# Performance work log

Measured on AMD Instinct MI355X. Metric: run time of the kernel, lower is better.

The kernel has to match this reference:

```python
import jax, jax.numpy as jnp
import numpy as np
import math

# model / graph sizes
N_NODES, N_EDGES = 50000, 400000
IN_DIM, N_HID = 256, 128
NUM_TYPES, NUM_REL = 4, 5
N_HEADS, D_K = 4, 32
N_LAYERS, MAX_LEN = 2, 240
SQRT_DK = math.sqrt(D_K)


def _gelu(x):
    return jax.nn.gelu(x, approximate=False)  # torch F.gelu is exact erf


def _per_type_linear(x, types, W, b):
    # x:[n,din], types:[n] int, W:[T,din,dout], b:[T,dout]
    out = jnp.zeros((x.shape[0], W.shape[-1]), x.dtype)
    for t in range(W.shape[0]):  # small fixed type count
        out = jnp.where((types == t)[:, None], x @ W[t] + b[t], out)
    return out


def setup_inputs() -> dict:
    key = jax.random.key(0)
    ks = jax.random.split(key, 16)
    node_feature = jax.random.normal(ks[0], (N_NODES, IN_DIM), jnp.float32)
    node_type = jax.random.randint(ks[1], (N_NODES,), 0, NUM_TYPES)
    edge_index = jax.random.randint(ks[2], (2, N_EDGES), 0, N_NODES)
    edge_type = jax.random.randint(ks[3], (N_EDGES,), 0, NUM_REL)
    edge_time = jax.random.randint(ks[4], (N_EDGES,), 0, MAX_LEN)

    def w(k, shape, s=0.05):
        return jax.random.normal(k, shape, jnp.float32) * s

    adapt_W = w(ks[5], (NUM_TYPES, IN_DIM, N_HID))
    adapt_b = jnp.zeros((NUM_TYPES, N_HID), jnp.float32)
    Wk = w(ks[6], (N_LAYERS, NUM_TYPES, N_HID, N_HID))
    Wq = w(ks[7], (N_LAYERS, NUM_TYPES, N_HID, N_HID))
    Wv = w(ks[8], (N_LAYERS, NUM_TYPES, N_HID, N_HID))
    Wa = w(ks[9], (N_LAYERS, NUM_TYPES, N_HID, N_HID))
    bk = jnp.zeros((N_LAYERS, NUM_TYPES, N_HID), jnp.float32)
    bq = jnp.zeros((N_LAYERS, NUM_TYPES, N_HID), jnp.float32)
    bv = jnp.zeros((N_LAYERS, NUM_TYPES, N_HID), jnp.float32)
    ba = jnp.zeros((N_LAYERS, NUM_TYPES, N_HID), jnp.float32)
    rel_pri = jnp.ones((N_LAYERS, NUM_REL, N_HEADS), jnp.float32)
    rel_att = w(ks[10], (N_LAYERS, NUM_REL, N_HEADS, D_K, D_K), 0.1) + jnp.eye(D_K, dtype=jnp.float32)
    rel_msg = w(ks[11], (N_LAYERS, NUM_REL, N_HEADS, D_K, D_K), 0.1) + jnp.eye(D_K, dtype=jnp.float32)
    skip = jnp.ones((N_LAYERS, NUM_TYPES), jnp.float32)
    # fixed sinusoidal RTE table (pyHGT RelTemporalEncoding, requires_grad=False)
    pos = np.arange(MAX_LEN, dtype=np.float32)[:, None]
    div = np.exp(np.arange(0, N_HID, 2, dtype=np.float32) * -(math.log(10000.0) / N_HID))
    tab = np.zeros((MAX_LEN, N_HID), np.float32)
    tab[:, 0::2] = np.sin(pos * div) / math.sqrt(N_HID)
    tab[:, 1::2] = np.cos(pos * div) / math.sqrt(N_HID)
    rte_emb = jnp.asarray(tab)
    rte_W = w(ks[12], (N_LAYERS, N_HID, N_HID))
    rte_b = jnp.zeros((N_LAYERS, N_HID), jnp.float32)
    return dict(node_feature=node_feature, adapt_W=adapt_W, adapt_b=adapt_b,
                Wk=Wk, bk=bk, Wq=Wq, bq=bq, Wv=Wv, bv=bv, Wa=Wa, ba=ba,
                rel_pri=rel_pri, rel_att=rel_att, rel_msg=rel_msg, skip=skip,
                rte_emb=rte_emb, rte_W=rte_W, rte_b=rte_b,
                node_type=node_type, edge_index=edge_index,
                edge_type=edge_type, edge_time=edge_time)


def reference(node_feature, adapt_W, adapt_b, Wk, bk, Wq, bq, Wv, bv, Wa, ba,
              rel_pri, rel_att, rel_msg, skip, rte_emb, rte_W, rte_b,
              node_type, edge_index, edge_type, edge_time):
    n = node_feature.shape[0]
    src, dst = edge_index[0], edge_index[1]  # PyG: row0 = source j, row1 = target i
    st, tt = node_type[src], node_type[dst]
    # per-type input adaptation (all types use Linear + GELU)
    h = _gelu(_per_type_linear(node_feature, node_type, adapt_W, adapt_b))  # [N, n_hid]
    for l in range(N_LAYERS):  # HGTConv stack
        x_j, x_i = h[src], h[dst]
        s_e = x_j + rte_emb[edge_time] @ rte_W[l] + rte_b[l]  # RTE on source per edge
        k = _per_type_linear(s_e, st, Wk[l], bk[l]).reshape(-1, N_HEADS, D_K)
        v = _per_type_linear(s_e, st, Wv[l], bv[l]).reshape(-1, N_HEADS, D_K)
        q = _per_type_linear(x_i, tt, Wq[l], bq[l]).reshape(-1, N_HEADS, D_K)
        att = jnp.zeros((k.shape[0], N_HEADS), h.dtype)
        msg = jnp.zeros_like(v)
        for r in range(NUM_REL):  # small fixed relation count
            m = edge_type == r
            kr = jnp.einsum('ehd,hdk->ehk', k, rel_att[l, r])
            ar = jnp.einsum('ehd,ehd->eh', q, kr) * rel_pri[l, r] / SQRT_DK
            mr = jnp.einsum('ehd,hdk->ehk', v, rel_msg[l, r])
            att = jnp.where(m[:, None], ar, att)
            msg = jnp.where(m[:, None, None], mr, msg)
        # segment softmax over incoming edges of each target node
        amax = jax.lax.stop_gradient(jax.ops.segment_max(att, dst, num_segments=n))
        ex = jnp.exp(att - amax[dst])
        denom = jax.ops.segment_sum(ex, dst, num_segments=n)
        alpha = ex / (denom[dst] + 1e-16)
        aggr = jax.ops.segment_sum((msg * alpha[:, :, None]).reshape(-1, N_HEADS * D_K),
                                   dst, num_segments=n)  # [N, n_hid]
        g = _gelu(aggr)
        res = jnp.zeros_like(h)
        for t in range(NUM_TYPES):  # per-type output transform + gated skip
            a_t = jax.nn.sigmoid(skip[l, t])
            res = jnp.where((node_type == t)[:, None],
                            (g @ Wa[l, t] + ba[l, t]) * a_t + h * (1.0 - a_t), res)
        h = res
    return h
```

## Files before the change

### kernel.cpp

```cpp
#include <hip/hip_runtime.h>
#include <math.h>

#define NN     50000
#define NE     400000
#define INDIM  256
#define NH     128
#define NTYPE  4
#define NREL   5
#define NHEAD  4
#define DK     32
#define RSQRT_DK 0.17677669529663687f
#define BN     64
#define NSCAN_BLK ((NN + 255) / 256)
#define XB     260

__device__ __forceinline__ float gelu_f(float x){
    return 0.5f * x * (1.0f + erff(x * 0.70710678118654752f));
}

__device__ __forceinline__ void gload16(const float* g, float* s){
    __builtin_amdgcn_global_load_lds(
        (const __attribute__((address_space(1))) void*)g,
        (__attribute__((address_space(3))) void*)s, 16, 0, 0);
}

__global__ void GNN_nscatter(const int* __restrict__ ntype, int* __restrict__ ncur,
                             int* __restrict__ nperm){
    __shared__ int lcnt[4], lbase[4];
    int tid = threadIdx.x;
    if (tid < 4) lcnt[tid] = 0;
    __syncthreads();
    int n = blockIdx.x * 256 + tid;
    int t = 0, lpos = 0;
    bool ok = (n < NN);
    if (ok){ t = ntype[n]; lpos = atomicAdd(&lcnt[t], 1); }
    __syncthreads();
    if (tid < 4 && lcnt[tid] > 0) lbase[tid] = atomicAdd(&ncur[tid], lcnt[tid]);
    __syncthreads();
    if (ok) nperm[t * NN + lbase[t] + lpos] = n;
}

__global__ void GNN_deg(const int* __restrict__ edst, int* __restrict__ deg){
    int e = blockIdx.x * 256 + threadIdx.x;
    if (e < NE) atomicAdd(&deg[edst[e]], 1);
}

__global__ void GNN_scan1(const int* __restrict__ deg, int* __restrict__ rowptr,
                          int* __restrict__ bsum){
    __shared__ int s[256];
    int g = blockIdx.x * 256 + threadIdx.x;
    int v = (g < NN) ? deg[g] : 0;
    s[threadIdx.x] = v;
    __syncthreads();
    for (int off = 1; off < 256; off <<= 1){
        int t = (threadIdx.x >= off) ? s[threadIdx.x - off] : 0;
        __syncthreads();
        s[threadIdx.x] += t;
        __syncthreads();
    }
    if (g < NN) rowptr[g] = s[threadIdx.x] - v;
    if (threadIdx.x == 255) bsum[blockIdx.x] = s[255];
}

__global__ void GNN_scan2(const int* __restrict__ bsum, int* __restrict__ bbase){
    __shared__ int s[256];
    int v = (threadIdx.x < NSCAN_BLK) ? bsum[threadIdx.x] : 0;
    s[threadIdx.x] = v;
    __syncthreads();
    for (int off = 1; off < 256; off <<= 1){
        int t = (threadIdx.x >= off) ? s[threadIdx.x - off] : 0;
        __syncthreads();
        s[threadIdx.x] += t;
        __syncthreads();
    }
    bbase[threadIdx.x] = s[threadIdx.x] - v;
}

__global__ void GNN_scan3(int* __restrict__ rowptr, const int* __restrict__ bbase){
    int g = blockIdx.x * 256 + threadIdx.x;
    if (g < NN) rowptr[g] += bbase[blockIdx.x];
    if (g == 0) rowptr[NN] = NE;
}

__global__ void GNN_csr_scatter(const int* __restrict__ edst, const int* __restrict__ rowptr,
                                int* __restrict__ cursor, int* __restrict__ csr_e){
    int e = blockIdx.x * 256 + threadIdx.x;
    if (e >= NE) return;
    int d = edst[e];
    int pos = atomicAdd(&cursor[d], 1);
    csr_e[rowptr[d] + pos] = e;
}

template<int MODE>
__device__ __forceinline__ void gemm_tile(
    const float* __restrict__ X, int K,
    const float* __restrict__ W, const float* __restrict__ brow,
    float a_t, const float* __restrict__ Hprev,
    float* Xs, float* Ws, const int* nids,
    float* __restrict__ OUT)
{
    int tid = threadIdx.x;
    int cq = tid & 31, rq = tid >> 5;

    int xc0 = tid >> 6,          xr0i = tid & 63;
    int xc1 = (256 + tid) >> 6,  xr1i = tid & 63;
    int nid0 = nids[xr0i], nid1 = nids[xr1i];
    const float* xp0 = (nid0 >= 0) ? X + (size_t)nid0 * K + xc0 * 4 : nullptr;
    const float* xp1 = (nid1 >= 0) ? X + (size_t)nid1 * K + xc1 * 4 : nullptr;
    int wk = tid >> 5, wc4 = (tid & 31) * 4;

    float4 xr0, xr1, wr0, wr1, wr2, wr3;
    const float4 z4 = make_float4(0.f, 0.f, 0.f, 0.f);

    #define LOADREGS(k0)                                                        \
        xr0 = xp0 ? *(const float4*)(xp0 + (k0)) : z4;                          \
        xr1 = xp1 ? *(const float4*)(xp1 + (k0)) : z4;                          \
        wr0 = *(const float4*)(W + (size_t)((k0) + wk     ) * NH + wc4);        \
        wr1 = *(const float4*)(W + (size_t)((k0) + wk +  8) * NH + wc4);        \
        wr2 = *(const float4*)(W + (size_t)((k0) + wk + 16) * NH + wc4);        \
        wr3 = *(const float4*)(W + (size_t)((k0) + wk + 24) * NH + wc4);

    #define WRITELDS()                                                          \
        *(float4*)&Xs[xc0 * XB + xr0i * 4] = xr0;                               \
        *(float4*)&Xs[xc1 * XB + xr1i * 4] = xr1;                               \
        *(float4*)&Ws[(wk     ) * 128 + wc4] = wr0;                             \
        *(float4*)&Ws[(wk +  8) * 128 + wc4] = wr1;                             \
        *(float4*)&Ws[(wk + 16) * 128 + wc4] = wr2;                             \
        *(float4*)&Ws[(wk + 24) * 128 + wc4] = wr3;

    float acc[8][4];
    #pragma unroll
    for (int i = 0; i < 8; i++){ acc[i][0]=0.f; acc[i][1]=0.f; acc[i][2]=0.f; acc[i][3]=0.f; }

    LOADREGS(0);
    for (int k0 = 0; k0 < K; k0 += 32){
        WRITELDS();
        __syncthreads();
        if (k0 + 32 < K){ LOADREGS(k0 + 32); }
        #pragma unroll 2
        for (int c4 = 0; c4 < 8; c4++){
            float4 w0 = *(const float4*)&Ws[(c4*4+0)*128 + cq*4];
            float4 w1 = *(const float4*)&Ws[(c4*4+1)*128 + cq*4];
            float4 w2 = *(const float4*)&Ws[(c4*4+2)*128 + cq*4];
            float4 w3 = *(const float4*)&Ws[(c4*4+3)*128 + cq*4];
            #pragma unroll
            for (int i = 0; i < 8; i++){
                float4 xv = *(const float4*)&Xs[c4 * XB + (rq + 8*i) * 4];
                acc[i][0] += xv.x*w0.x + xv.y*w1.x + xv.z*w2.x + xv.w*w3.x;
                acc[i][1] += xv.x*w0.y + xv.y*w1.y + xv.z*w2.y + xv.w*w3.y;
                acc[i][2] += xv.x*w0.z + xv.y*w1.z + xv.z*w2.z + xv.w*w3.z;
                acc[i][3] += xv.x*w0.w + xv.y*w1.w + xv.z*w2.w + xv.w*w3.w;
            }
        }
        __syncthreads();
    }
    #undef LOADREGS
    #undef WRITELDS

    float4 b4 = *(const float4*)(brow + cq * 4);
    float one_m = 1.f - a_t;
    #pragma unroll
    for (int i = 0; i < 8; i++){
        int r = rq + 8*i;
        int nid = nids[r];
        if (nid < 0) continue;
        float v0 = acc[i][0] + b4.x, v1 = acc[i][1] + b4.y;
        float v2 = acc[i][2] + b4.z, v3 = acc[i][3] + b4.w;
        if (MODE == 0){ v0 = gelu_f(v0); v1 = gelu_f(v1); v2 = gelu_f(v2); v3 = gelu_f(v3); }
        if (MODE == 2){
            float4 hp = *(const float4*)(Hprev + (size_t)nid * NH + cq * 4);
            v0 = v0 * a_t + hp.x * one_m; v1 = v1 * a_t + hp.y * one_m;
            v2 = v2 * a_t + hp.z * one_m; v3 = v3 * a_t + hp.w * one_m;
        }
        *(float4*)(OUT + (size_t)nid * NH + cq * 4) = make_float4(v0, v1, v2, v3);
    }
}

template<int MODE>
__device__ __forceinline__ void gemm_tile_dma(
    const float* __restrict__ X, int K,
    const float* __restrict__ W, const float* __restrict__ brow,
    float a_t, const float* __restrict__ Hprev,
    float* Xs, float* Ws, const int* nids,
    float* __restrict__ OUT)
{
    int tid = threadIdx.x;
    int cq = tid & 31, rq = tid >> 5;
    int lane = tid & 63, w = tid >> 6;

    int nidl = nids[lane]; if (nidl < 0) nidl = 0;
    const float* xrow  = X + (size_t)nidl * K;
    const float* wbase = W + lane * 4;

    float acc[8][4];
    #pragma unroll
    for (int i = 0; i < 8; i++){ acc[i][0]=0.f; acc[i][1]=0.f; acc[i][2]=0.f; acc[i][3]=0.f; }

    #define STAGE(k0, Xb, Wb)                                                   \
        gload16(xrow + (k0) + w * 4,       (Xb) + w * 256);                     \
        gload16(xrow + (k0) + (w + 4) * 4, (Xb) + (w + 4) * 256);               \
        gload16(wbase + (size_t)((k0) + 2 * (w     )) * NH, (Wb) + (w     ) * 256); \
        gload16(wbase + (size_t)((k0) + 2 * (w +  4)) * NH, (Wb) + (w +  4) * 256); \
        gload16(wbase + (size_t)((k0) + 2 * (w +  8)) * NH, (Wb) + (w +  8) * 256); \
        gload16(wbase + (size_t)((k0) + 2 * (w + 12)) * NH, (Wb) + (w + 12) * 256);

    STAGE(0, Xs, Ws);
    int buf = 0;
    for (int k0 = 0; k0 < K; k0 += 32){
        __syncthreads();
        if (k0 + 32 < K){
            float* Xn = Xs + (buf ^ 1) * 2048;
            float* Wn = Ws + (buf ^ 1) * 4096;
            STAGE(k0 + 32, Xn, Wn);
        }
        const float* Xsb = Xs + buf * 2048;
        const float* Wsb = Ws + buf * 4096;
        #pragma unroll 2
        for (int c4 = 0; c4 < 8; c4++){
            float4 w0 = *(const float4*)&Wsb[(c4*4+0)*128 + cq*4];
            float4 w1 = *(const float4*)&Wsb[(c4*4+1)*128 + cq*4];
            float4 w2 = *(const float4*)&Wsb[(c4*4+2)*128 + cq*4];
            float4 w3 = *(const float4*)&Wsb[(c4*4+3)*128 + cq*4];
            #pragma unroll
            for (int i = 0; i < 8; i++){
                float4 xv = *(const float4*)&Xsb[c4 * 256 + (rq + 8*i) * 4];
                acc[i][0] += xv.x*w0.x + xv.y*w1.x + xv.z*w2.x + xv.w*w3.x;
                acc[i][1] += xv.x*w0.y + xv.y*w1.y + xv.z*w2.y + xv.w*w3.y;
                acc[i][2] += xv.x*w0.z + xv.y*w1.z + xv.z*w2.z + xv.w*w3.z;
                acc[i][3] += xv.x*w0.w + xv.y*w1.w + xv.z*w2.w + xv.w*w3.w;
            }
        }
        __syncthreads();
        buf ^= 1;
    }
    #undef STAGE

    float4 b4 = *(const float4*)(brow + cq * 4);
    float one_m = 1.f - a_t;
    #pragma unroll
    for (int i = 0; i < 8; i++){
        int r = rq + 8*i;
        int nid = nids[r];
        if (nid < 0) continue;
        float v0 = acc[i][0] + b4.x, v1 = acc[i][1] + b4.y;
        float v2 = acc[i][2] + b4.z, v3 = acc[i][3] + b4.w;
        if (MODE == 0){ v0 = gelu_f(v0); v1 = gelu_f(v1); v2 = gelu_f(v2); v3 = gelu_f(v3); }
        if (MODE == 2){
            float4 hp = *(const float4*)(Hprev + (size_t)nid * NH + cq * 4);
            v0 = v0 * a_t + hp.x * one_m; v1 = v1 * a_t + hp.y * one_m;
            v2 = v2 * a_t + hp.z * one_m; v3 = v3 * a_t + hp.w * one_m;
        }
        *(float4*)(OUT + (size_t)nid * NH + cq * 4) = make_float4(v0, v1, v2, v3);
    }
}

template<int MODE>
__global__ __launch_bounds__(256) void GNN_ptype_gemm(
    const float* __restrict__ X, int K,
    const float* __restrict__ Wall, const float* __restrict__ ball,
    const float* __restrict__ skiprow, const float* __restrict__ Hprev,
    const int* __restrict__ nperm, const int* __restrict__ counts,
    float* __restrict__ OUT)
{
    int t = blockIdx.y;
    int cnt = counts[t];
    int rbase = blockIdx.x * BN;
    if (rbase >= cnt) return;
    __shared__ float Xs[2 * 2048];
    __shared__ float Ws[2 * 4096];
    __shared__ int nids[BN];
    int tid = threadIdx.x;
    if (tid < BN){
        int idx = rbase + tid;
        nids[tid] = (idx < cnt) ? nperm[t * NN + idx] : -1;
    }
    __syncthreads();
    float a_t = 0.f;
    if (MODE == 2) a_t = 1.f / (1.f + expf(-skiprow[t]));
    gemm_tile_dma<MODE>(X, K, Wall + (size_t)t * K * NH, ball + t * NH,
                        a_t, Hprev, Xs, Ws, nids, OUT);
}

__global__ __launch_bounds__(256) void GNN_qkv_gemm(
    const float* __restrict__ X,
    const float* __restrict__ Wq, const float* __restrict__ bq,
    const float* __restrict__ Wk, const float* __restrict__ bk,
    const float* __restrict__ Wv, const float* __restrict__ bv,
    const int* __restrict__ nperm, const int* __restrict__ counts,
    float* __restrict__ Qn, float* __restrict__ Kn, float* __restrict__ Vn)
{
    int t = blockIdx.y;
    int cnt = counts[t];
    int rbase = blockIdx.x * BN;
    if (rbase >= cnt) return;
    __shared__ float Xs[8 * XB];
    __shared__ float Ws[32 * 128];
    __shared__ int nids[BN];
    int tid = threadIdx.x;
    if (tid < BN){
        int idx = rbase + tid;
        nids[tid] = (idx < cnt) ? nperm[t * NN + idx] : -1;
    }
    __syncthreads();
    int z = blockIdx.z;
    const float* W = (z == 0) ? Wq : (z == 1) ? Wk : Wv;
    const float* b = (z == 0) ? bq : (z == 1) ? bk : bv;
    float* OUT     = (z == 0) ? Qn : (z == 1) ? Kn : Vn;
    gemm_tile<1>(X, NH, W + (size_t)t * NH * NH, b + t * NH,
                 0.f, nullptr, Xs, Ws, nids, OUT);
}

__global__ void GNN_rte_tab(const float* __restrict__ rte_emb, const float* __restrict__ rW,
                            const float* __restrict__ rb, float* __restrict__ tab){
    int m = blockIdx.x, j = threadIdx.x;
    __shared__ float e[NH];
    e[j] = rte_emb[m * NH + j];
    __syncthreads();
    float a = rb[j];
    #pragma unroll 8
    for (int d = 0; d < NH; d++) a += e[d] * rW[d * NH + j];
    tab[m * NH + j] = a;
}

__global__ void GNN_rte_proj(const float* __restrict__ tab, const float* __restrict__ WkL,
                             const float* __restrict__ WvL, float* __restrict__ RK,
                             float* __restrict__ RV){
    int m = blockIdx.x, j = threadIdx.x;
    int sel = blockIdx.y; int t = sel >> 1; int which = sel & 1;
    const float* W = (which ? WvL : WkL) + (size_t)t * NH * NH;
    float* O = which ? RV : RK;
    __shared__ float e[NH];
    e[j] = tab[m * NH + j];
    __syncthreads();
    float a = 0.f;
    #pragma unroll 8
    for (int d = 0; d < NH; d++) a += e[d] * W[d * NH + j];
    O[(size_t)(t * 240 + m) * NH + j] = a;
}

__global__ __launch_bounds__(256) void GNN_qa(
    const float* __restrict__ Qn, const float* __restrict__ relA, float* __restrict__ QA)
{
    __shared__ float Atp[4 * 1072];
    int r = blockIdx.y;
    int nb = blockIdx.x * 64;
    int tid = threadIdx.x;
    const float* Ar = relA + (size_t)r * NHEAD * DK * DK;
    for (int x = tid; x < NHEAD * DK * DK; x += 256){
        int hh = x >> 10, rem = x & 1023, dd = rem >> 5, cc = rem & 31;
        Atp[hh * 1072 + (dd >> 2) * 132 + cc * 4 + (dd & 3)] = Ar[x];
    }
    __syncthreads();
    int cq = tid & 31, rq = tid >> 5;
    int h = cq >> 3;
    int abase = h * 1072 + (cq & 7) * 132;
    int rowoff[8];
    #pragma unroll
    for (int i = 0; i < 8; i++){
        int node = nb + rq + 8*i;
        if (node >= NN) node = NN - 1;
        rowoff[i] = node * NH + h * 32;
    }
    float acc[8][4];
    #pragma unroll
    for (int i = 0; i < 8; i++){ acc[i][0]=0.f; acc[i][1]=0.f; acc[i][2]=0.f; acc[i][3]=0.f; }
    #pragma unroll 2
    for (int c4 = 0; c4 < 8; c4++){
        float4 av0 = *(const float4*)&Atp[abase + c4 * 16 + 0];
        float4 av1 = *(const float4*)&Atp[abase + c4 * 16 + 4];
        float4 av2 = *(const float4*)&Atp[abase + c4 * 16 + 8];
        float4 av3 = *(const float4*)&Atp[abase + c4 * 16 + 12];
        #pragma unroll
        for (int i = 0; i < 8; i++){
            float4 qv = *(const float4*)(Qn + rowoff[i] + c4 * 4);
            acc[i][0] += qv.x*av0.x + qv.y*av1.x + qv.z*av2.x + qv.w*av3.x;
            acc[i][1] += qv.x*av0.y + qv.y*av1.y + qv.z*av2.y + qv.w*av3.y;
            acc[i][2] += qv.x*av0.z + qv.y*av1.z + qv.z*av2.z + qv.w*av3.z;
            acc[i][3] += qv.x*av0.w + qv.y*av1.w + qv.z*av2.w + qv.w*av3.w;
        }
    }
    #pragma unroll
    for (int i = 0; i < 8; i++){
        int node = nb + rq + 8*i;
        if (node >= NN) continue;
        *(float4*)(QA + ((size_t)r * NN + node) * NH + cq * 4) =
            make_float4(acc[i][0], acc[i][1], acc[i][2], acc[i][3]);
    }
}

__global__ __launch_bounds__(256) void GNN_edge_att(
    const float* __restrict__ Kn, const float* __restrict__ RK, const float* __restrict__ QA,
    const int* __restrict__ esrc, const int* __restrict__ edst,
    const int* __restrict__ etype, const int* __restrict__ etime,
    const int* __restrict__ ntype, const float* __restrict__ relP,
    float* __restrict__ att)
{
    int tid = threadIdx.x;
    int e = blockIdx.x * 8 + (tid >> 5);
    if (e >= NE) return;
    int lane = tid & 31;
    int s = esrc[e], d = edst[e], r = etype[e], tm = etime[e];
    int st = ntype[s];
    float4 k4 = *(const float4*)(Kn + (size_t)s * NH + lane * 4);
    float4 rk = *(const float4*)(RK + (size_t)(st * 240 + tm) * NH + lane * 4);
    float4 qa = *(const float4*)(QA + ((size_t)r * NN + d) * NH + lane * 4);
    float pv = (k4.x + rk.x) * qa.x + (k4.y + rk.y) * qa.y
             + (k4.z + rk.z) * qa.z + (k4.w + rk.w) * qa.w;
    pv += __shfl_xor(pv, 4);
    pv += __shfl_xor(pv, 2);
    pv += __shfl_xor(pv, 1);
    if ((lane & 7) == 0){
        int head = lane >> 3;
        att[(size_t)e * NHEAD + head] = pv * relP[r * NHEAD + head] * RSQRT_DK;
    }
}

__global__ __launch_bounds__(256) void GNN_node_aggr(
    const float* __restrict__ att, const float* __restrict__ Vn, const float* __restrict__ RV,
    const int* __restrict__ rowptr, const int* __restrict__ csr_e,
    const int* __restrict__ esrc, const int* __restrict__ etype,
    const int* __restrict__ etime, const int* __restrict__ ntype,
    float* __restrict__ P)
{
    int tid = threadIdx.x;
    int i = blockIdx.x * 8 + (tid >> 5);
    if (i >= NN) return;
    int lane = tid & 31;
    int head = lane >> 3;
    int beg = rowptr[i], end = rowptr[i + 1];
    float mx = -3.4e38f;
    for (int k = beg; k < end; k++){
        int e = csr_e[k];
        mx = fmaxf(mx, att[(size_t)e * NHEAD + head]);
    }
    float4 acc[NREL];
    #pragma unroll
    for (int rr = 0; rr < NREL; rr++) acc[rr] = make_float4(0.f, 0.f, 0.f, 0.f);
    float den = 0.f;
    for (int k = beg; k < end; k++){
        int e = csr_e[k];
        int s = esrc[e], r = etype[e], tm = etime[e];
        int st = ntype[s];
        float ex = expf(att[(size_t)e * NHEAD + head] - mx);
        den += ex;
        float4 v4 = *(const float4*)(Vn + (size_t)s * NH + lane * 4);
        float4 rv = *(const float4*)(RV + (size_t)(st * 240 + tm) * NH + lane * 4);
        float vx = v4.x + rv.x, vy = v4.y + rv.y, vz = v4.z + rv.z, vw = v4.w + rv.w;
        #pragma unroll
        for (int rr = 0; rr < NREL; rr++){
            float w = (rr == r) ? ex : 0.f;
            acc[rr].x += w * vx; acc[rr].y += w * vy;
            acc[rr].z += w * vz; acc[rr].w += w * vw;
        }
    }
    float inv = 1.f / (den + 1e-16f);
    #pragma unroll
    for (int rr = 0; rr < NREL; rr++){
        *(float4*)(P + ((size_t)rr * NN + i) * NH + lane * 4) =
            make_float4(acc[rr].x * inv, acc[rr].y * inv, acc[rr].z * inv, acc[rr].w * inv);
    }
}

__global__ __launch_bounds__(256) void GNN_pm(
    const float* __restrict__ P, const float* __restrict__ relM, float* __restrict__ aggr)
{
    __shared__ float Msp[2][4 * 1072];
    int tid = threadIdx.x;
    int nb = blockIdx.x * 64;
    int cq = tid & 31, rq = tid >> 5;
    int h = cq >> 3;
    int mbase = h * 1072 + (cq & 7) * 132;
    int rowoff[8];
    #pragma unroll
    for (int i = 0; i < 8; i++){
        int node = nb + rq + 8*i;
        if (node >= NN) node = NN - 1;
        rowoff[i] = node * NH + h * 32;
    }
    float acc[8][4];
    #pragma unroll
    for (int i = 0; i < 8; i++){ acc[i][0]=0.f; acc[i][1]=0.f; acc[i][2]=0.f; acc[i][3]=0.f; }

    #pragma unroll
    for (int j = 0; j < 4; j++){
        int s = tid + 256 * j;
        float4 mv = *(const float4*)(relM + 4 * s);
        *(float4*)&Msp[0][(s >> 8) * 1072 + (s & 7) * 132 + ((s >> 3) & 31) * 4] = mv;
    }
    __syncthreads();

    #pragma unroll
    for (int r = 0; r < NREL; r++){
        float4 mpre[4];
        if (r + 1 < NREL){
            const float* Mn = relM + (size_t)(r + 1) * NHEAD * DK * DK;
            #pragma unroll
            for (int j = 0; j < 4; j++)
                mpre[j] = *(const float4*)(Mn + 4 * (tid + 256 * j));
        }
        const float* Ms = Msp[r & 1];
        const float* Pr = P + (size_t)r * NN * NH;
        #pragma unroll 2
        for (int d4 = 0; d4 < 8; d4++){
            float4 mv0 = *(const float4*)&Ms[mbase + d4 * 16 + 0];
            float4 mv1 = *(const float4*)&Ms[mbase + d4 * 16 + 4];
            float4 mv2 = *(const float4*)&Ms[mbase + d4 * 16 + 8];
            float4 mv3 = *(const float4*)&Ms[mbase + d4 * 16 + 12];
            #pragma unroll
            for (int i = 0; i < 8; i++){
                float4 pv = *(const float4*)(Pr + rowoff[i] + d4 * 4);
                acc[i][0] += pv.x*mv0.x + pv.y*mv1.x + pv.z*mv2.x + pv.w*mv3.x;
                acc[i][1] += pv.x*mv0.y + pv.y*mv1.y + pv.z*mv2.y + pv.w*mv3.y;
                acc[i][2] += pv.x*mv0.z + pv.y*mv1.z + pv.z*mv2.z + pv.w*mv3.z;
                acc[i][3] += pv.x*mv0.w + pv.y*mv1.w + pv.z*mv2.w + pv.w*mv3.w;
            }
        }
        if (r + 1 < NREL){
            #pragma unroll
            for (int j = 0; j < 4; j++){
                int s = tid + 256 * j;
                *(float4*)&Msp[(r + 1) & 1][(s >> 8) * 1072 + (s & 7) * 132 +
                                            ((s >> 3) & 31) * 4] = mpre[j];
            }
            __syncthreads();
        }
    }
    #pragma unroll
    for (int i = 0; i < 8; i++){
        int node = nb + rq + 8*i;
        if (node >= NN) continue;
        *(float4*)(aggr + (size_t)node * NH + cq * 4) =
            make_float4(gelu_f(acc[i][0]), gelu_f(acc[i][1]),
                        gelu_f(acc[i][2]), gelu_f(acc[i][3]));
    }
}

extern "C" void kernel_launch(void* const* d_in, const int* in_sizes, int n_in,
                              void* d_out, int out_size, void* d_ws, size_t ws_size,
                              hipStream_t stream)
{
    const float* node_feature = (const float*)d_in[0];
    const float* adapt_W = (const float*)d_in[1];
    const float* adapt_b = (const float*)d_in[2];
    const float* Wk = (const float*)d_in[3];
    const float* bk = (const float*)d_in[4];
    const float* Wq = (const float*)d_in[5];
    const float* bq = (const float*)d_in[6];
    const float* Wv = (const float*)d_in[7];
    const float* bv = (const float*)d_in[8];
    const float* Wa = (const float*)d_in[9];
    const float* ba = (const float*)d_in[10];
    const float* rel_pri = (const float*)d_in[11];
    const float* rel_att = (const float*)d_in[12];
    const float* rel_msg = (const float*)d_in[13];
    const float* skip = (const float*)d_in[14];
    const float* rte_emb = (const float*)d_in[15];
    const float* rte_W = (const float*)d_in[16];
    const float* rte_b = (const float*)d_in[17];
    const int* node_type = (const int*)d_in[18];
    const int* edge_index = (const int*)d_in[19];
    const int* edge_type = (const int*)d_in[20];
    const int* edge_time = (const int*)d_in[21];
    const int* esrc = edge_index;
    const int* edst = edge_index + NE;

    char* p = (char*)d_ws;
    auto alloc = [&](size_t bytes) -> char* {
        char* r = p; p += (bytes + 255) & ~(size_t)255; return r;
    };
    float* hA    = (float*)alloc((size_t)NN * NH * 4);
    float* Qn    = (float*)alloc((size_t)NN * NH * 4);
    float* Kn    = (float*)alloc((size_t)NN * NH * 4);
    float* Vn    = (float*)alloc((size_t)NN * NH * 4);
    float* QA    = (float*)alloc((size_t)NREL * NN * NH * 4);
    float* rtab  = (float*)alloc((size_t)240 * NH * 4);
    float* RK    = (float*)alloc((size_t)NTYPE * 240 * NH * 4);
    float* RV    = (float*)alloc((size_t)NTYPE * 240 * NH * 4);
    int* nperm   = (int*)alloc((size_t)NTYPE * NN * 4);
    int* rowptr  = (int*)alloc((size_t)(NN + 1) * 4);
    int* csr_e   = (int*)alloc((size_t)NE * 4);
    int* deg     = (int*)alloc((size_t)2 * NN * 4);
    int* cursor  = deg + NN;
    int* bsum    = (int*)alloc(256 * 4);
    int* bbase   = (int*)alloc(256 * 4);
    int* ncur    = (int*)alloc(64);
    float* att   = Qn;
    float* Pbuf  = QA;
    float* aggr  = Kn;

    hipMemsetAsync(ncur, 0, 64, stream);
    hipMemsetAsync(deg, 0, (size_t)2 * NN * 4, stream);

    GNN_nscatter<<<(NN + 255) / 256, 256, 0, stream>>>(node_type, ncur, nperm);
    GNN_deg<<<(NE + 255) / 256, 256, 0, stream>>>(edst, deg);
    GNN_scan1<<<NSCAN_BLK, 256, 0, stream>>>(deg, rowptr, bsum);
    GNN_scan2<<<1, 256, 0, stream>>>(bsum, bbase);
    GNN_scan3<<<NSCAN_BLK, 256, 0, stream>>>(rowptr, bbase);
    GNN_csr_scatter<<<(NE + 255) / 256, 256, 0, stream>>>(edst, rowptr, cursor, csr_e);

    dim3 ggrid((NN + BN - 1) / BN, NTYPE);
    GNN_ptype_gemm<0><<<ggrid, 256, 0, stream>>>(node_feature, INDIM, adapt_W, adapt_b,
                                                 nullptr, nullptr, nperm, ncur, hA);
    const float* hin = hA;
    for (int l = 0; l < 2; l++){
        const float* WkL = Wk + (size_t)l * NTYPE * NH * NH;
        const float* WqL = Wq + (size_t)l * NTYPE * NH * NH;
        const float* WvL = Wv + (size_t)l * NTYPE * NH * NH;
        const float* WaL = Wa + (size_t)l * NTYPE * NH * NH;
        const float* bkL = bk + (size_t)l * NTYPE * NH;
        const float* bqL = bq + (size_t)l * NTYPE * NH;
        const float* bvL = bv + (size_t)l * NTYPE * NH;
        const float* baL = ba + (size_t)l * NTYPE * NH;
        const float* relA = rel_att + (size_t)l * NREL * NHEAD * DK * DK;
        const float* relM = rel_msg + (size_t)l * NREL * NHEAD * DK * DK;
        const float* relP = rel_pri + (size_t)l * NREL * NHEAD;

        GNN_rte_tab<<<240, 128, 0, stream>>>(rte_emb, rte_W + (size_t)l * NH * NH,
                                             rte_b + (size_t)l * NH, rtab);
        GNN_rte_proj<<<dim3(240, NTYPE * 2), 128, 0, stream>>>(rtab, WkL, WvL, RK, RV);

        GNN_qkv_gemm<<<dim3(ggrid.x, NTYPE, 3), 256, 0, stream>>>(
            hin, WqL, bqL, WkL, bkL, WvL, bvL, nperm, ncur, Qn, Kn, Vn);

        GNN_qa<<<dim3((NN + 63) / 64, NREL), 256, 0, stream>>>(Qn, relA, QA);

        GNN_edge_att<<<(NE + 7) / 8, 256, 0, stream>>>(
            Kn, RK, QA, esrc, edst, edge_type, edge_time, node_type, relP, att);

        GNN_node_aggr<<<(NN + 7) / 8, 256, 0, stream>>>(
            att, Vn, RV, rowptr, csr_e, esrc, edge_type, edge_time, node_type, Pbuf);

        GNN_pm<<<(NN + 63) / 64, 256, 0, stream>>>(Pbuf, relM, aggr);

        float* hout = (l == 0) ? hA : (float*)d_out;
        GNN_ptype_gemm<2><<<ggrid, 256, 0, stream>>>(
            aggr, NH, WaL, baL, skip + (size_t)l * NTYPE, hin,
            nperm, ncur, hout);
        hin = hout;
    }
}
```

Measured before the change: 1.160 ms.

## Halve per-type GEMM row tile and stage through registers instead of DMA

```diff
diff --git a/kernel.cpp b/kernel.cpp
--- a/kernel.cpp
+++ b/kernel.cpp
@@ -11,17 +11,13 @@
 #define DK     32
 #define RSQRT_DK 0.17677669529663687f
 #define BN     64
+#define BN2    32
 #define NSCAN_BLK ((NN + 255) / 256)
 #define XB     260
+#define XB2    132
 
 __device__ __forceinline__ float gelu_f(float x){
     return 0.5f * x * (1.0f + erff(x * 0.70710678118654752f));
-}
-
-__device__ __forceinline__ void gload16(const float* g, float* s){
-    __builtin_amdgcn_global_load_lds(
-        (const __attribute__((address_space(1))) void*)g,
-        (__attribute__((address_space(3))) void*)s, 16, 0, 0);
 }
 
 __global__ void GNN_nscatter(const int* __restrict__ ntype, int* __restrict__ ncur,
@@ -177,7 +173,7 @@
 }
 
 template<int MODE>
-__device__ __forceinline__ void gemm_tile_dma(
+__device__ __forceinline__ void gemm_tile32(
     const float* __restrict__ X, int K,
     const float* __restrict__ W, const float* __restrict__ brow,
     float a_t, const float* __restrict__ Hprev,
@@ -186,44 +182,47 @@
 {
     int tid = threadIdx.x;
     int cq = tid & 31, rq = tid >> 5;
-    int lane = tid & 63, w = tid >> 6;
-
-    int nidl = nids[lane]; if (nidl < 0) nidl = 0;
-    const float* xrow  = X + (size_t)nidl * K;
-    const float* wbase = W + lane * 4;
-
-    float acc[8][4];
-    #pragma unroll
-    for (int i = 0; i < 8; i++){ acc[i][0]=0.f; acc[i][1]=0.f; acc[i][2]=0.f; acc[i][3]=0.f; }
-
-    #define STAGE(k0, Xb, Wb)                                                   \
-        gload16(xrow + (k0) + w * 4,       (Xb) + w * 256);                     \
-        gload16(xrow + (k0) + (w + 4) * 4, (Xb) + (w + 4) * 256);               \
-        gload16(wbase + (size_t)((k0) + 2 * (w     )) * NH, (Wb) + (w     ) * 256); \
-        gload16(wbase + (size_t)((k0) + 2 * (w +  4)) * NH, (Wb) + (w +  4) * 256); \
-        gload16(wbase + (size_t)((k0) + 2 * (w +  8)) * NH, (Wb) + (w +  8) * 256); \
-        gload16(wbase + (size_t)((k0) + 2 * (w + 12)) * NH, (Wb) + (w + 12) * 256);
-
-    STAGE(0, Xs, Ws);
-    int buf = 0;
+
+    int nid0 = nids[tid & 31];
+    const float* xp0 = (nid0 >= 0) ? X + (size_t)nid0 * K + (tid >> 5) * 4 : nullptr;
+    int wk = tid >> 5, wc4 = (tid & 31) * 4;
+    int xdst = (tid >> 5) * XB2 + (tid & 31) * 4;
+
+    float4 xr0, wr0, wr1, wr2, wr3;
+    const float4 z4 = make_float4(0.f, 0.f, 0.f, 0.f);
+
+    #define LOADREGS2(k0)                                                       \
+        xr0 = xp0 ? *(const float4*)(xp0 + (k0)) : z4;                          \
+        wr0 = *(const float4*)(W + (size_t)((k0) + wk     ) * NH + wc4);        \
+        wr1 = *(const float4*)(W + (size_t)((k0) + wk +  8) * NH + wc4);        \
+        wr2 = *(const float4*)(W + (size_t)((k0) + wk + 16) * NH + wc4);        \
+        wr3 = *(const float4*)(W + (size_t)((k0) + wk + 24) * NH + wc4);
+
+    #define WRITELDS2()                                                         \
+        *(float4*)&Xs[xdst] = xr0;                                              \
+        *(float4*)&Ws[(wk     ) * 128 + wc4] = wr0;                             \
+        *(float4*)&Ws[(wk +  8) * 128 + wc4] = wr1;                             \
+        *(float4*)&Ws[(wk + 16) * 128 + wc4] = wr2;                             \
+        *(float4*)&Ws[(wk + 24) * 128 + wc4] = wr3;
+
+    float acc[4][4];
+    #pragma unroll
+    for (int i = 0; i < 4; i++){ acc[i][0]=0.f; acc[i][1]=0.f; acc[i][2]=0.f; acc[i][3]=0.f; }
+
+    LOADREGS2(0);
     for (int k0 = 0; k0 < K; k0 += 32){
-        __syncthreads();
-        if (k0 + 32 < K){
-            float* Xn = Xs + (buf ^ 1) * 2048;
-            float* Wn = Ws + (buf ^ 1) * 4096;
-            STAGE(k0 + 32, Xn, Wn);
-        }
-        const float* Xsb = Xs + buf * 2048;
-        const float* Wsb = Ws + buf * 4096;
+        WRITELDS2();
+        __syncthreads();
+        if (k0 + 32 < K){ LOADREGS2(k0 + 32); }
         #pragma unroll 2
         for (int c4 = 0; c4 < 8; c4++){
-            float4 w0 = *(const float4*)&Wsb[(c4*4+0)*128 + cq*4];
-            float4 w1 = *(const float4*)&Wsb[(c4*4+1)*128 + cq*4];
-            float4 w2 = *(const float4*)&Wsb[(c4*4+2)*128 + cq*4];
-            float4 w3 = *(const float4*)&Wsb[(c4*4+3)*128 + cq*4];
+            float4 w0 = *(const float4*)&Ws[(c4*4+0)*128 + cq*4];
+            float4 w1 = *(const float4*)&Ws[(c4*4+1)*128 + cq*4];
+            float4 w2 = *(const float4*)&Ws[(c4*4+2)*128 + cq*4];
+            float4 w3 = *(const float4*)&Ws[(c4*4+3)*128 + cq*4];
             #pragma unroll
-            for (int i = 0; i < 8; i++){
-                float4 xv = *(const float4*)&Xsb[c4 * 256 + (rq + 8*i) * 4];
+            for (int i = 0; i < 4; i++){
+                float4 xv = *(const float4*)&Xs[c4 * XB2 + (rq + 8*i) * 4];
                 acc[i][0] += xv.x*w0.x + xv.y*w1.x + xv.z*w2.x + xv.w*w3.x;
                 acc[i][1] += xv.x*w0.y + xv.y*w1.y + xv.z*w2.y + xv.w*w3.y;
                 acc[i][2] += xv.x*w0.z + xv.y*w1.z + xv.z*w2.z + xv.w*w3.z;
@@ -231,14 +230,14 @@
             }
         }
         __syncthreads();
-        buf ^= 1;
-    }
-    #undef STAGE
+    }
+    #undef LOADREGS2
+    #undef WRITELDS2
 
     float4 b4 = *(const float4*)(brow + cq * 4);
     float one_m = 1.f - a_t;
     #pragma unroll
-    for (int i = 0; i < 8; i++){
+    for (int i = 0; i < 4; i++){
         int r = rq + 8*i;
         int nid = nids[r];
         if (nid < 0) continue;
@@ -264,21 +263,21 @@
 {
     int t = blockIdx.y;
     int cnt = counts[t];
-    int rbase = blockIdx.x * BN;
+    int rbase = blockIdx.x * BN2;
     if (rbase >= cnt) return;
-    __shared__ float Xs[2 * 2048];
-    __shared__ float Ws[2 * 4096];
-    __shared__ int nids[BN];
-    int tid = threadIdx.x;
-    if (tid < BN){
+    __shared__ float Xs[8 * XB2];
+    __shared__ float Ws[32 * 128];
+    __shared__ int nids[BN2];
+    int tid = threadIdx.x;
+    if (tid < BN2){
         int idx = rbase + tid;
         nids[tid] = (idx < cnt) ? nperm[t * NN + idx] : -1;
     }
     __syncthreads();
     float a_t = 0.f;
     if (MODE == 2) a_t = 1.f / (1.f + expf(-skiprow[t]));
-    gemm_tile_dma<MODE>(X, K, Wall + (size_t)t * K * NH, ball + t * NH,
-                        a_t, Hprev, Xs, Ws, nids, OUT);
+    gemm_tile32<MODE>(X, K, Wall + (size_t)t * K * NH, ball + t * NH,
+                      a_t, Hprev, Xs, Ws, nids, OUT);
 }
 
 __global__ __launch_bounds__(256) void GNN_qkv_gemm(
@@ -598,8 +597,9 @@
     GNN_scan3<<<NSCAN_BLK, 256, 0, stream>>>(rowptr, bbase);
     GNN_csr_scatter<<<(NE + 255) / 256, 256, 0, stream>>>(edst, rowptr, cursor, csr_e);
 
-    dim3 ggrid((NN + BN - 1) / BN, NTYPE);
-    GNN_ptype_gemm<0><<<ggrid, 256, 0, stream>>>(node_feature, INDIM, adapt_W, adapt_b,
+    dim3 pgrid((NN + BN2 - 1) / BN2, NTYPE);
+    dim3 qgrid((NN + BN - 1) / BN, NTYPE, 3);
+    GNN_ptype_gemm<0><<<pgrid, 256, 0, stream>>>(node_feature, INDIM, adapt_W, adapt_b,
                                                  nullptr, nullptr, nperm, ncur, hA);
     const float* hin = hA;
     for (int l = 0; l < 2; l++){
@@ -619,7 +619,7 @@
                                              rte_b + (size_t)l * NH, rtab);
         GNN_rte_proj<<<dim3(240, NTYPE * 2), 128, 0, stream>>>(rtab, WkL, WvL, RK, RV);
 
-        GNN_qkv_gemm<<<dim3(ggrid.x, NTYPE, 3), 256, 0, stream>>>(
+        GNN_qkv_gemm<<<qgrid, 256, 0, stream>>>(
             hin, WqL, bqL, WkL, bkL, WvL, bvL, nperm, ncur, Qn, Kn, Vn);
 
         GNN_qa<<<dim3((NN + 63) / 64, NREL), 256, 0, stream>>>(Qn, relA, QA);
@@ -633,7 +633,7 @@
         GNN_pm<<<(NN + 63) / 64, 256, 0, stream>>>(Pbuf, relM, aggr);
 
         float* hout = (l == 0) ? hA : (float*)d_out;
-        GNN_ptype_gemm<2><<<ggrid, 256, 0, stream>>>(
+        GNN_ptype_gemm<2><<<pgrid, 256, 0, stream>>>(
             aggr, NH, WaL, baL, skip + (size_t)l * NTYPE, hin,
             nperm, ncur, hout);
         hin = hout;
```

Measured after the change: 1.099 ms. -5.3%, faster.
